# Kernel optimization log

Measured on AMD Instinct MI355X. Metric: run time of the kernel, lower is better.

## Reference

```python
import jax, jax.numpy as jnp
import numpy as np

B, T, C, E = 4, 2048, 1024, 8  # batch, seq, n_embd, num_experts


def setup_inputs() -> dict:
    key = jax.random.key(0)
    k_x, k_wr, k_we = jax.random.split(key, 3)
    x = jax.random.normal(k_x, (B, T, C), dtype=jnp.float32)
    # router: Linear(C, E); scale chosen so softmax gates spread around the 0.5 threshold
    Wr = jax.random.normal(k_wr, (E, C), dtype=jnp.float32) * 0.05
    br = jnp.zeros((E,), dtype=jnp.float32)
    # experts: E x Linear(C, C), y = x @ W^T + b
    We = jax.random.normal(k_we, (E, C, C), dtype=jnp.float32) * (1.0 / np.sqrt(C))
    be = jnp.zeros((E, C), dtype=jnp.float32)
    return {"x": x, "Wr": Wr, "br": br, "We": We, "be": be}


def reference(x, Wr, br, We, be):
    # router logits + softmax gates: [B, T, E]
    logits = jnp.einsum('btc,ec->bte', x, Wr) + br
    gates = jax.nn.softmax(logits, axis=-1)
    # hard selection: token goes through expert e iff gate_e > 0.5 (at most one
    # expert per token since gates sum to 1); output is NOT scaled by the gate.
    mask = (gates > 0.5).astype(x.dtype)  # [B, T, E]
    # all-expert outputs (torch Linear: y = x @ W^T + b): [B, T, E, C]
    h = jnp.einsum('btc,edc->bted', x, We) + be
    # masked combine -> [B, T, C]; unrouted tokens stay zero like torch.zeros_like
    return jnp.einsum('bted,bte->btd', h, mask)
```

## Files before the change

### kernel.cpp

```cpp
#include <hip/hip_runtime.h>
#include <hip/hip_bf16.h>
#include <stdint.h>

#define NB 4
#define NT 2048
#define NC 1024
#define NE 8
#define NTOK (NB * NT)
#define MAXT (NTOK / 128 + NE - 1)
#define CSTRIDE 32

typedef __attribute__((ext_vector_type(4))) float floatx4;
typedef __attribute__((ext_vector_type(8))) __bf16 bf16x8;
typedef __attribute__((ext_vector_type(4))) __bf16 bf16x4;
typedef unsigned short ushort_t;

#define AS1 __attribute__((address_space(1)))
#define AS3 __attribute__((address_space(3)))

__device__ __forceinline__ ushort_t f2bf(float f) {
    uint32_t u = __builtin_bit_cast(uint32_t, f);
    u += 0x7FFFu + ((u >> 16) & 1u);
    return (ushort_t)(u >> 16);
}

__global__ void zero_counts_k(int* __restrict__ counts) {
    if (threadIdx.x < NE) counts[threadIdx.x * CSTRIDE] = 0;
}

__global__ __launch_bounds__(256, 4) void router_k(
    const float* __restrict__ x, const float* __restrict__ Wr,
    const float* __restrict__ br, float* __restrict__ out,
    int* __restrict__ counts, int* __restrict__ buckets,
    ushort_t* __restrict__ xbf ,
    const float* __restrict__ We, ushort_t* __restrict__ webf )
{
    const int wave = threadIdx.x >> 6;
    const int lane = threadIdx.x & 63;
    const int tok  = blockIdx.x * 4 + wave;

    if (webf) {
        const size_t cbase = ((size_t)(blockIdx.x * 256 + threadIdx.x)) * 8;
        {
            float4 a = *(const float4*)(We + cbase);
            float4 b = *(const float4*)(We + cbase + 4);
            union { bf16x8 v; ushort_t s[8]; } p;
            p.s[0] = f2bf(a.x); p.s[1] = f2bf(a.y); p.s[2] = f2bf(a.z); p.s[3] = f2bf(a.w);
            p.s[4] = f2bf(b.x); p.s[5] = f2bf(b.y); p.s[6] = f2bf(b.z); p.s[7] = f2bf(b.w);
            *(bf16x8*)(webf + cbase) = p.v;
        }
        {
            float4 a = *(const float4*)(We + cbase + 4194304);
            float4 b = *(const float4*)(We + cbase + 4194304 + 4);
            union { bf16x8 v; ushort_t s[8]; } p;
            p.s[0] = f2bf(a.x); p.s[1] = f2bf(a.y); p.s[2] = f2bf(a.z); p.s[3] = f2bf(a.w);
            p.s[4] = f2bf(b.x); p.s[5] = f2bf(b.y); p.s[6] = f2bf(b.z); p.s[7] = f2bf(b.w);
            *(bf16x8*)(webf + cbase + 4194304) = p.v;
        }
    }

    const float4* xr = (const float4*)(x + (size_t)tok * NC);
    float4 xv[4];
#pragma unroll
    for (int j = 0; j < 4; ++j) xv[j] = xr[lane + 64 * j];

    float acc[NE];
#pragma unroll
    for (int e = 0; e < NE; ++e) {
        const float4* wr = (const float4*)(Wr + e * NC);
        float a = 0.f;
#pragma unroll
        for (int j = 0; j < 4; ++j) {
            float4 w = wr[lane + 64 * j];
            a += xv[j].x * w.x; a += xv[j].y * w.y;
            a += xv[j].z * w.z; a += xv[j].w * w.w;
        }
        acc[e] = a;
    }
#pragma unroll
    for (int off = 32; off >= 1; off >>= 1)
#pragma unroll
        for (int e = 0; e < NE; ++e) acc[e] += __shfl_xor(acc[e], off);

#pragma unroll
    for (int e = 0; e < NE; ++e) acc[e] += br[e];

    float lmax = acc[0]; int emax = 0;
#pragma unroll
    for (int e = 1; e < NE; ++e) if (acc[e] > lmax) { lmax = acc[e]; emax = e; }
    float S = 0.f;
#pragma unroll
    for (int e = 0; e < NE; ++e) S += expf(acc[e] - lmax);

    const bool routed = (S < 2.0f);
    if (routed) {
        if (xbf) {
            union { bf16x4 v; ushort_t s[4]; } p;
#pragma unroll
            for (int j = 0; j < 4; ++j) {
                p.s[0] = f2bf(xv[j].x); p.s[1] = f2bf(xv[j].y);
                p.s[2] = f2bf(xv[j].z); p.s[3] = f2bf(xv[j].w);
                *(bf16x4*)(xbf + (size_t)tok * NC + (lane + 64 * j) * 4) = p.v;
            }
        }
        if (lane == 0) {
            int pos = atomicAdd(&counts[emax * CSTRIDE], 1);
            buckets[emax * NTOK + pos] = tok;
        }
    } else {
        float4 z = make_float4(0.f, 0.f, 0.f, 0.f);
        float4* orow = (float4*)(out + (size_t)tok * NC);
#pragma unroll
        for (int j = 0; j < 4; ++j) orow[lane + 64 * j] = z;
    }
}

__device__ __forceinline__ void gload_lds16(const void* g, void* l) {
    __builtin_amdgcn_global_load_lds((const AS1 unsigned int*)g,
                                     (AS3 unsigned int*)l, 16, 0, 0);
}

__global__ __launch_bounds__(256) void moe_gemm_bf16_k(
    const ushort_t* __restrict__ xbf, const ushort_t* __restrict__ webf,
    const float* __restrict__ be, float* __restrict__ out,
    const int* __restrict__ counts, const int* __restrict__ buckets)
{
    int cw[NE];
#pragma unroll
    for (int i = 0; i < NE; ++i) cw[i] = counts[i * CSTRIDE];
    const int t = blockIdx.x;
    int base = 0, e = -1, m0 = 0;
#pragma unroll
    for (int i = 0; i < NE; ++i) {
        const int te = (cw[i] + 127) >> 7;
        if (e < 0 && t < base + te) { e = i; m0 = (t - base) << 7; }
        base += te;
    }
    if (e < 0) return;
    const int cnt = cw[e];
    const int n0  = blockIdx.y * 128;

    __shared__ ushort_t As[128 * 64];
    __shared__ ushort_t Bs[128 * 64];

    const int tid   = threadIdx.x;
    const int wave  = tid >> 6, lane = tid & 63;
    const int chunk = tid & 7;
    const int rbase = tid >> 3;

    const ushort_t* asrc[4];
    const ushort_t* bsrc[4];
#pragma unroll
    for (int i = 0; i < 4; ++i) {
        const int row = i * 32 + rbase;
        const int sc  = chunk ^ (row & 7);
        int mi = m0 + row; if (mi >= cnt) mi = cnt - 1;
        const int tok = buckets[e * NTOK + mi];
        asrc[i] = xbf + (size_t)tok * NC + sc * 8;
        bsrc[i] = webf + ((size_t)(e * 1024 + n0 + row)) * NC + sc * 8;
    }

    const int wm = (wave >> 1) * 64, wn = (wave & 1) * 64;
    const int fr = lane & 15, hi = lane >> 4;

    floatx4 acc[4][4];
#pragma unroll
    for (int m = 0; m < 4; ++m)
#pragma unroll
        for (int n = 0; n < 4; ++n) acc[m][n] = (floatx4)(0.0f);

    for (int k0 = 0; k0 < NC; k0 += 64) {
#pragma unroll
        for (int i = 0; i < 4; ++i)
            gload_lds16(asrc[i] + k0, &As[(i * 256 + tid) * 8]);
#pragma unroll
        for (int i = 0; i < 4; ++i)
            gload_lds16(bsrc[i] + k0, &Bs[(i * 256 + tid) * 8]);
        __syncthreads();
#pragma unroll
        for (int ks = 0; ks < 2; ++ks) {
            bf16x8 af[4], bfv[4];
#pragma unroll
            for (int m = 0; m < 4; ++m) {
                const int row = wm + m * 16 + fr;
                const int cg  = (ks * 4 + hi) ^ (row & 7);
                af[m] = *(const bf16x8*)((const char*)As + row * 128 + cg * 16);
            }
#pragma unroll
            for (int n = 0; n < 4; ++n) {
                const int row = wn + n * 16 + fr;
                const int cg  = (ks * 4 + hi) ^ (row & 7);
                bfv[n] = *(const bf16x8*)((const char*)Bs + row * 128 + cg * 16);
            }
#pragma unroll
            for (int m = 0; m < 4; ++m)
#pragma unroll
                for (int n = 0; n < 4; ++n)
                    acc[m][n] = __builtin_amdgcn_mfma_f32_16x16x32_bf16(
                        af[m], bfv[n], acc[m][n], 0, 0, 0);
        }
        __syncthreads();
    }

    const int r4 = (lane >> 4) * 4;
    float bev[4];
#pragma unroll
    for (int n = 0; n < 4; ++n) bev[n] = be[e * NC + n0 + wn + n * 16 + fr];
#pragma unroll
    for (int m = 0; m < 4; ++m) {
#pragma unroll
        for (int j = 0; j < 4; ++j) {
            const int trow = m0 + wm + m * 16 + r4 + j;
            if (trow < cnt) {
                const int tok = buckets[e * NTOK + trow];
                float* orow = out + (size_t)tok * NC + n0 + wn + fr;
#pragma unroll
                for (int n = 0; n < 4; ++n) orow[n * 16] = acc[m][n][j] + bev[n];
            }
        }
    }
}

#define BM 64
#define BN 64
#define BK 32
#define LPAD 40
__global__ __launch_bounds__(256) void moe_gemm_k(
    const float* __restrict__ x, const float* __restrict__ We,
    const float* __restrict__ be, float* __restrict__ out,
    const int* __restrict__ counts, const int* __restrict__ buckets)
{
    const int e   = blockIdx.z;
    const int cnt = counts[e * CSTRIDE];
    const int m0  = blockIdx.x * BM;
    if (m0 >= cnt) return;
    const int n0  = blockIdx.y * BN;

    __shared__ ushort_t As[BM * LPAD];
    __shared__ ushort_t Bs[BM * LPAD];

    const int tid  = threadIdx.x;
    const int srow = tid >> 2;
    const int scg  = (tid & 3) * 8;

    const int mrow = m0 + srow;
    const int tokA = (mrow < cnt) ? buckets[e * NTOK + mrow] : -1;
    const float* xrow = x + (size_t)(tokA < 0 ? 0 : tokA) * NC;
    const float* wrow = We + ((size_t)e * NC + (n0 + srow)) * NC;

    const int wave = tid >> 6, lane = tid & 63;
    const int wm = (wave >> 1) * 32, wn = (wave & 1) * 32;
    const int fr = lane & 15;
    const int fk = (lane >> 4) * 8;

    floatx4 acc[2][2];
#pragma unroll
    for (int m = 0; m < 2; ++m)
#pragma unroll
        for (int n = 0; n < 2; ++n) acc[m][n] = (floatx4)(0.0f);

    for (int k0 = 0; k0 < NC; k0 += BK) {
        float4 a0 = make_float4(0.f,0.f,0.f,0.f), a1 = a0;
        if (tokA >= 0) {
            a0 = *(const float4*)(xrow + k0 + scg);
            a1 = *(const float4*)(xrow + k0 + scg + 4);
        }
        float4 b0 = *(const float4*)(wrow + k0 + scg);
        float4 b1 = *(const float4*)(wrow + k0 + scg + 4);

        __syncthreads();
        union { bf16x8 v; ushort_t s[8]; } pa, pb;
        pa.s[0] = f2bf(a0.x); pa.s[1] = f2bf(a0.y); pa.s[2] = f2bf(a0.z); pa.s[3] = f2bf(a0.w);
        pa.s[4] = f2bf(a1.x); pa.s[5] = f2bf(a1.y); pa.s[6] = f2bf(a1.z); pa.s[7] = f2bf(a1.w);
        pb.s[0] = f2bf(b0.x); pb.s[1] = f2bf(b0.y); pb.s[2] = f2bf(b0.z); pb.s[3] = f2bf(b0.w);
        pb.s[4] = f2bf(b1.x); pb.s[5] = f2bf(b1.y); pb.s[6] = f2bf(b1.z); pb.s[7] = f2bf(b1.w);
        *(bf16x8*)&As[srow * LPAD + scg] = pa.v;
        *(bf16x8*)&Bs[srow * LPAD + scg] = pb.v;
        __syncthreads();

        bf16x8 af[2], bfr[2];
#pragma unroll
        for (int m = 0; m < 2; ++m)
            af[m] = *(const bf16x8*)&As[(wm + m * 16 + fr) * LPAD + fk];
#pragma unroll
        for (int n = 0; n < 2; ++n)
            bfr[n] = *(const bf16x8*)&Bs[(wn + n * 16 + fr) * LPAD + fk];
#pragma unroll
        for (int m = 0; m < 2; ++m)
#pragma unroll
            for (int n = 0; n < 2; ++n)
                acc[m][n] = __builtin_amdgcn_mfma_f32_16x16x32_bf16(af[m], bfr[n], acc[m][n], 0, 0, 0);
    }

    const int r4 = (lane >> 4) * 4;
#pragma unroll
    for (int m = 0; m < 2; ++m) {
        const int trowb = m0 + wm + m * 16 + r4;
#pragma unroll
        for (int j = 0; j < 4; ++j) {
            const int trow = trowb + j;
            if (trow < cnt) {
                const int tok = buckets[e * NTOK + trow];
#pragma unroll
                for (int n = 0; n < 2; ++n) {
                    const int d = n0 + wn + n * 16 + fr;
                    out[(size_t)tok * NC + d] = acc[m][n][j] + be[e * NC + d];
                }
            }
        }
    }
}

extern "C" void kernel_launch(void* const* d_in, const int* in_sizes, int n_in,
                              void* d_out, int out_size, void* d_ws, size_t ws_size,
                              hipStream_t stream)
{
    const float* x  = (const float*)d_in[0];
    const float* Wr = (const float*)d_in[1];
    const float* br = (const float*)d_in[2];
    const float* We = (const float*)d_in[3];
    const float* be = (const float*)d_in[4];
    float* out = (float*)d_out;

    int* counts  = (int*)d_ws;
    int* buckets = (int*)((char*)d_ws + 1024);
    const size_t XBF_OFF = 263168;
    const size_t WBF_OFF = 17040384;
    const size_t WS_NEED = 33817600;
    const bool fast = (ws_size >= WS_NEED);

    ushort_t* xbf  = fast ? (ushort_t*)((char*)d_ws + XBF_OFF) : nullptr;
    ushort_t* webf = fast ? (ushort_t*)((char*)d_ws + WBF_OFF) : nullptr;

    hipLaunchKernelGGL(zero_counts_k, dim3(1), dim3(64), 0, stream, counts);
    hipLaunchKernelGGL(router_k, dim3(NTOK / 4), dim3(256), 0, stream,
                       x, Wr, br, out, counts, buckets, xbf, We, webf);
    if (fast) {
        hipLaunchKernelGGL(moe_gemm_bf16_k, dim3(MAXT, NC / 128, 1), dim3(256),
                           0, stream, xbf, webf, be, out, counts, buckets);
    } else {
        hipLaunchKernelGGL(moe_gemm_k, dim3(NTOK / BM, NC / BN, NE), dim3(256),
                           0, stream, x, We, be, out, counts, buckets);
    }
}
```

Measured before the change: 57.82 us.

## Split router into LDS-tiled token blocks and separate weight-conversion blocks

The fused router now launches 128 router blocks, each handling 64 tokens by tiling x and Wr through LDS, plus 2048 dedicated blocks that only convert expert weights to bf16. Before, 2048 blocks each did four tokens and also a slice of weight conversion. The aim is to reuse each Wr load across many tokens and to separate the bandwidth-bound conversion from the router math. It also converts every token of x to bf16, not just routed ones, which adds write traffic. Only 128 router blocks may underuse the GPU while they run the serial K loop.

New measurement: 74.86 us. +29.5%, slower.

```diff
diff --git a/kernel.cpp b/kernel.cpp
--- a/kernel.cpp
+++ b/kernel.cpp
@@ -9,6 +9,10 @@
 #define NTOK (NB * NT)
 #define MAXT (NTOK / 128 + NE - 1)
 #define CSTRIDE 32
+#define RTB 128
+#define TPB 64
+#define KC 128
+#define XS_STRIDE 130
 
 typedef __attribute__((ext_vector_type(4))) float floatx4;
 typedef __attribute__((ext_vector_type(8))) __bf16 bf16x8;
@@ -28,19 +32,18 @@
     if (threadIdx.x < NE) counts[threadIdx.x * CSTRIDE] = 0;
 }
 
-__global__ __launch_bounds__(256, 4) void router_k(
+__global__ __launch_bounds__(256, 4) void router_conv_k(
     const float* __restrict__ x, const float* __restrict__ Wr,
     const float* __restrict__ br, float* __restrict__ out,
     int* __restrict__ counts, int* __restrict__ buckets,
-    ushort_t* __restrict__ xbf ,
-    const float* __restrict__ We, ushort_t* __restrict__ webf )
+    ushort_t* __restrict__ xbf,
+    const float* __restrict__ We, ushort_t* __restrict__ webf)
 {
-    const int wave = threadIdx.x >> 6;
-    const int lane = threadIdx.x & 63;
-    const int tok  = blockIdx.x * 4 + wave;
-
-    if (webf) {
-        const size_t cbase = ((size_t)(blockIdx.x * 256 + threadIdx.x)) * 8;
+    const int bid = blockIdx.x;
+
+    if (bid >= RTB) {
+        const int cb = bid - RTB;
+        const size_t cbase = ((size_t)(cb * 256 + threadIdx.x)) * 8;
         {
             float4 a = *(const float4*)(We + cbase);
             float4 b = *(const float4*)(We + cbase + 4);
@@ -57,7 +60,96 @@
             p.s[4] = f2bf(b.x); p.s[5] = f2bf(b.y); p.s[6] = f2bf(b.z); p.s[7] = f2bf(b.w);
             *(bf16x8*)(webf + cbase + 4194304) = p.v;
         }
-    }
+        return;
+    }
+
+    __shared__ float xs[TPB * XS_STRIDE];
+    __shared__ float wrs[NE * KC];
+    __shared__ float lg[TPB * NE];
+    __shared__ int   tinfo[TPB];
+
+    const int tid  = threadIdx.x;
+    const int e    = tid >> 5, l = tid & 31;
+    const int tb   = bid * TPB;
+    const int srow = tid >> 2, spart = tid & 3;
+
+    float acc0 = 0.f, acc1 = 0.f;
+
+    for (int k0 = 0; k0 < NC; k0 += KC) {
+        __syncthreads();
+        {
+            const float* src = x + (size_t)(tb + srow) * NC + k0 + spart * 32;
+            float*       dst = &xs[srow * XS_STRIDE + spart * 32];
+            ushort_t*    xd  = xbf + (size_t)(tb + srow) * NC + k0 + spart * 32;
+#pragma unroll
+            for (int j = 0; j < 8; ++j) {
+                float4 v = *(const float4*)(src + 4 * j);
+                *(float2*)(dst + 4 * j)     = make_float2(v.x, v.y);
+                *(float2*)(dst + 4 * j + 2) = make_float2(v.z, v.w);
+                union { bf16x4 vb; ushort_t s[4]; } p;
+                p.s[0] = f2bf(v.x); p.s[1] = f2bf(v.y);
+                p.s[2] = f2bf(v.z); p.s[3] = f2bf(v.w);
+                *(bf16x4*)(xd + 4 * j) = p.vb;
+            }
+        }
+        {
+            float4 wv = *(const float4*)(Wr + e * NC + k0 + l * 4);
+            *(float4*)(&wrs[e * KC + l * 4]) = wv;
+        }
+        __syncthreads();
+#pragma unroll 16
+        for (int k2 = 0; k2 < KC; k2 += 2) {
+            float2 w = *(const float2*)(&wrs[e * KC + k2]);
+            float2 a = *(const float2*)(&xs[l * XS_STRIDE + k2]);
+            float2 b = *(const float2*)(&xs[(l + 32) * XS_STRIDE + k2]);
+            acc0 += a.x * w.x; acc0 += a.y * w.y;
+            acc1 += b.x * w.x; acc1 += b.y * w.y;
+        }
+    }
+
+    lg[l * NE + e]        = acc0 + br[e];
+    lg[(l + 32) * NE + e] = acc1 + br[e];
+    __syncthreads();
+
+    if (tid < TPB) {
+        float v[NE];
+#pragma unroll
+        for (int i = 0; i < NE; ++i) v[i] = lg[tid * NE + i];
+        float lmax = v[0]; int emax = 0;
+#pragma unroll
+        for (int i = 1; i < NE; ++i) if (v[i] > lmax) { lmax = v[i]; emax = i; }
+        float S = 0.f;
+#pragma unroll
+        for (int i = 0; i < NE; ++i) S += expf(v[i] - lmax);
+        int info = -1;
+        if (S < 2.0f) {
+            info = emax;
+            int pos = atomicAdd(&counts[emax * CSTRIDE], 1);
+            buckets[emax * NTOK + pos] = tb + tid;
+        }
+        tinfo[tid] = info;
+    }
+    __syncthreads();
+
+    const int wv2 = tid >> 6, ln = tid & 63;
+    for (int t = wv2; t < TPB; t += 4) {
+        if (tinfo[t] < 0) {
+            float4 z = make_float4(0.f, 0.f, 0.f, 0.f);
+            float4* orow = (float4*)(out + (size_t)(tb + t) * NC);
+#pragma unroll
+            for (int j = 0; j < 4; ++j) orow[ln + 64 * j] = z;
+        }
+    }
+}
+
+__global__ __launch_bounds__(256, 4) void router_k(
+    const float* __restrict__ x, const float* __restrict__ Wr,
+    const float* __restrict__ br, float* __restrict__ out,
+    int* __restrict__ counts, int* __restrict__ buckets)
+{
+    const int wave = threadIdx.x >> 6;
+    const int lane = threadIdx.x & 63;
+    const int tok  = blockIdx.x * 4 + wave;
 
     const float4* xr = (const float4*)(x + (size_t)tok * NC);
     float4 xv[4];
@@ -81,7 +173,6 @@
     for (int off = 32; off >= 1; off >>= 1)
 #pragma unroll
         for (int e = 0; e < NE; ++e) acc[e] += __shfl_xor(acc[e], off);
-
 #pragma unroll
     for (int e = 0; e < NE; ++e) acc[e] += br[e];
 
@@ -92,17 +183,7 @@
 #pragma unroll
     for (int e = 0; e < NE; ++e) S += expf(acc[e] - lmax);
 
-    const bool routed = (S < 2.0f);
-    if (routed) {
-        if (xbf) {
-            union { bf16x4 v; ushort_t s[4]; } p;
-#pragma unroll
-            for (int j = 0; j < 4; ++j) {
-                p.s[0] = f2bf(xv[j].x); p.s[1] = f2bf(xv[j].y);
-                p.s[2] = f2bf(xv[j].z); p.s[3] = f2bf(xv[j].w);
-                *(bf16x4*)(xbf + (size_t)tok * NC + (lane + 64 * j) * 4) = p.v;
-            }
-        }
+    if (S < 2.0f) {
         if (lane == 0) {
             int pos = atomicAdd(&counts[emax * CSTRIDE], 1);
             buckets[emax * NTOK + pos] = tok;
@@ -329,16 +410,17 @@
     const size_t WS_NEED = 33817600;
     const bool fast = (ws_size >= WS_NEED);
 
-    ushort_t* xbf  = fast ? (ushort_t*)((char*)d_ws + XBF_OFF) : nullptr;
-    ushort_t* webf = fast ? (ushort_t*)((char*)d_ws + WBF_OFF) : nullptr;
-
     hipLaunchKernelGGL(zero_counts_k, dim3(1), dim3(64), 0, stream, counts);
-    hipLaunchKernelGGL(router_k, dim3(NTOK / 4), dim3(256), 0, stream,
-                       x, Wr, br, out, counts, buckets, xbf, We, webf);
     if (fast) {
+        ushort_t* xbf  = (ushort_t*)((char*)d_ws + XBF_OFF);
+        ushort_t* webf = (ushort_t*)((char*)d_ws + WBF_OFF);
+        hipLaunchKernelGGL(router_conv_k, dim3(RTB + 2048), dim3(256), 0, stream,
+                           x, Wr, br, out, counts, buckets, xbf, We, webf);
         hipLaunchKernelGGL(moe_gemm_bf16_k, dim3(MAXT, NC / 128, 1), dim3(256),
                            0, stream, xbf, webf, be, out, counts, buckets);
     } else {
+        hipLaunchKernelGGL(router_k, dim3(NTOK / 4), dim3(256), 0, stream,
+                           x, Wr, br, out, counts, buckets);
         hipLaunchKernelGGL(moe_gemm_k, dim3(NTOK / BM, NC / BN, NE), dim3(256),
                            0, stream, x, We, be, out, counts, buckets);
     }
```
